# Kernel tuning notes

Measured on AMD Instinct MI355X. Metric: run time of the kernel, lower is better.

The kernel has to match this reference:

```python
import jax, jax.numpy as jnp
import numpy as np

DIM = 768
HEADS = 12
HIDDEN = 3072  # dim * mlp_ratio
EPS = 1e-5


def layernorm(x, g, b):
    mu = jnp.mean(x, axis=-1, keepdims=True)
    var = jnp.var(x, axis=-1, keepdims=True)
    return (x - mu) * jax.lax.rsqrt(var + EPS) * g + b


def setup_inputs() -> dict:
    key = jax.random.key(0)
    ks = jax.random.split(key, 10)
    s = 0.02
    return {
        "x": jax.random.normal(ks[0], (4, 1024, DIM), jnp.float32),
        "attention_mask": jax.random.randint(ks[1], (4, 1024), 0, 2, jnp.int32),
        "ln1_g": jnp.ones((DIM,), jnp.float32),
        "ln1_b": jnp.zeros((DIM,), jnp.float32),
        "ln2_g": jnp.ones((DIM,), jnp.float32),
        "ln2_b": jnp.zeros((DIM,), jnp.float32),
        "w_qkv": jax.random.normal(ks[2], (DIM, 3 * DIM), jnp.float32) * s,
        "b_qkv": jnp.zeros((3 * DIM,), jnp.float32),
        "w_proj": jax.random.normal(ks[3], (DIM, DIM), jnp.float32) * s,
        "b_proj": jnp.zeros((DIM,), jnp.float32),
        "w_fc1": jax.random.normal(ks[4], (DIM, HIDDEN), jnp.float32) * s,
        "b_fc1": jnp.zeros((HIDDEN,), jnp.float32),
        "w_fc2": jax.random.normal(ks[5], (HIDDEN, DIM), jnp.float32) * s,
        "b_fc2": jnp.zeros((DIM,), jnp.float32),
    }


def reference(x, attention_mask, ln1_g, ln1_b, ln2_g, ln2_b,
              w_qkv, b_qkv, w_proj, b_proj, w_fc1, b_fc1, w_fc2, b_fc2):
    B, N, C = x.shape
    hd = C // HEADS
    scale = hd ** -0.5

    # --- attention branch ---
    h = layernorm(x, ln1_g, ln1_b)
    qkv = (h @ w_qkv + b_qkv).reshape(B, N, 3, HEADS, hd)
    q, k, v = qkv[:, :, 0], qkv[:, :, 1], qkv[:, :, 2]  # [B,N,H,hd]
    attn = jnp.einsum('bnhd,bmhd->bhnm', q, k) * scale
    mask_bias = jnp.where(attention_mask == 0, -10000.0, 0.0)[:, None, None, :]
    attn = jax.nn.softmax(attn + mask_bias, axis=-1)
    o = jnp.einsum('bhnm,bmhd->bnhd', attn, v).reshape(B, N, C)
    x = x + (o @ w_proj + b_proj)

    # --- MLP branch ---
    h = layernorm(x, ln2_g, ln2_b)
    h = jax.nn.gelu(h @ w_fc1 + b_fc1, approximate=False)
    x = x + (h @ w_fc2 + b_fc2)
    return x
```

## Files before the change

### kernel.cpp

```cpp
#include <hip/hip_runtime.h>

#define DIM 768
#define NTOK 4096
#define HID 3072

typedef __attribute__((ext_vector_type(8))) short bf16x8;
typedef __attribute__((ext_vector_type(4))) float f32x4;

__device__ inline unsigned short f2bf(float f){
  unsigned u = __float_as_uint(f);
  u += 0x7fff + ((u >> 16) & 1);
  return (unsigned short)(u >> 16);
}
__device__ inline unsigned cvt_pk_bf16(float a, float b){
  unsigned r;
  asm("v_cvt_pk_bf16_f32 %0, %1, %2" : "=v"(r) : "v"(a), "v"(b));
  return r;
}
__device__ inline void gload_lds16(const void* g, void* l){
  __builtin_amdgcn_global_load_lds(
      (const __attribute__((address_space(1))) unsigned int*)g,
      (__attribute__((address_space(3))) unsigned int*)l, 16, 0, 0);
}
template<int N> __device__ inline void wait_vmcnt(){
  if constexpr (N == 0) asm volatile("s_waitcnt vmcnt(0)" ::: "memory");
  else if constexpr (N == 2) asm volatile("s_waitcnt vmcnt(2)" ::: "memory");
  else if constexpr (N == 4) asm volatile("s_waitcnt vmcnt(4)" ::: "memory");
  else if constexpr (N == 6) asm volatile("s_waitcnt vmcnt(6)" ::: "memory");
  else if constexpr (N == 8) asm volatile("s_waitcnt vmcnt(8)" ::: "memory");
  else static_assert(N == 0, "unsupported vmcnt");
}
__device__ inline int swz_read(int row, int hi){
  return (row * 64 + hi * 16) ^ ((row & 7) << 4);
}

__global__ __launch_bounds__(256) void ln_kernel(const float* __restrict__ x,
    const float* __restrict__ g, const float* __restrict__ b,
    unsigned short* __restrict__ out)
{
  int row = blockIdx.x * 4 + (threadIdx.x >> 6);
  int lane = threadIdx.x & 63;
  const float* xr = x + (size_t)row * DIM;
  float4 v[3];
  float s = 0.f, s2 = 0.f;
#pragma unroll
  for (int j = 0; j < 3; ++j){
    v[j] = *(const float4*)(xr + j * 256 + lane * 4);
    s  += v[j].x + v[j].y + v[j].z + v[j].w;
    s2 += v[j].x*v[j].x + v[j].y*v[j].y + v[j].z*v[j].z + v[j].w*v[j].w;
  }
#pragma unroll
  for (int m = 1; m < 64; m <<= 1){ s += __shfl_xor(s, m, 64); s2 += __shfl_xor(s2, m, 64); }
  float mu  = s * (1.f / 768.f);
  float var = s2 * (1.f / 768.f) - mu * mu;
  float inv = rsqrtf(var + 1e-5f);
#pragma unroll
  for (int j = 0; j < 3; ++j){
    int c0 = j * 256 + lane * 4;
    float vv[4] = { v[j].x, v[j].y, v[j].z, v[j].w };
    ushort4 o4;
    o4.x = f2bf((vv[0] - mu) * inv * g[c0 + 0] + b[c0 + 0]);
    o4.y = f2bf((vv[1] - mu) * inv * g[c0 + 1] + b[c0 + 1]);
    o4.z = f2bf((vv[2] - mu) * inv * g[c0 + 2] + b[c0 + 2]);
    o4.w = f2bf((vv[3] - mu) * inv * g[c0 + 3] + b[c0 + 3]);
    *(ushort4*)(out + (size_t)row * DIM + c0) = o4;
  }
}

__global__ __launch_bounds__(256) void transpose4_kernel(
    const float* __restrict__ w_qkv, const float* __restrict__ w_proj,
    const float* __restrict__ w_fc1, const float* __restrict__ w_fc2,
    unsigned short* __restrict__ tq, unsigned short* __restrict__ tp,
    unsigned short* __restrict__ t1, unsigned short* __restrict__ t2)
{
  __shared__ __align__(16) unsigned short tile[32][33];
  int id = blockIdx.x;
  const float* W; unsigned short* Wt; int K, N, tx_n;
  if (id < 1728)      { W = w_qkv;  Wt = tq; K = 768;  N = 2304; tx_n = 72; }
  else if (id < 2304) { W = w_proj; Wt = tp; K = 768;  N = 768;  tx_n = 24; id -= 1728; }
  else if (id < 4608) { W = w_fc1;  Wt = t1; K = 768;  N = 3072; tx_n = 96; id -= 2304; }
  else                { W = w_fc2;  Wt = t2; K = 3072; N = 768;  tx_n = 24; id -= 4608; }
  int n0 = (id % tx_n) * 32, k0 = (id / tx_n) * 32;
  int tx = threadIdx.x & 31, ty = threadIdx.x >> 5;
#pragma unroll
  for (int i = 0; i < 32; i += 8)
    tile[ty + i][tx] = f2bf(W[(size_t)(k0 + ty + i) * N + n0 + tx]);
  __syncthreads();
#pragma unroll
  for (int i = 0; i < 32; i += 8)
    Wt[(size_t)(n0 + ty + i) * K + k0 + tx] = tile[tx][ty + i];
}

__global__ __launch_bounds__(256) void pack_mask_kernel(const int* __restrict__ am,
    unsigned long long* __restrict__ pm)
{
  int lane = threadIdx.x & 63, w = threadIdx.x >> 6, b = blockIdx.x;
  for (int k = w; k < 16; k += 4){
    unsigned long long m = __ballot(am[b * 1024 + k * 64 + lane] != 0);
    if (lane == 0) pm[b * 16 + k] = m;
  }
}

template<int DEPTH, int EPI, typename OutT>
__global__ __launch_bounds__(256) void gemm_kernel(
    const unsigned short* __restrict__ A,
    const unsigned short* __restrict__ Bt,
    const float* __restrict__ bias,
    const float* __restrict__ resid,
    OutT* __restrict__ C,
    unsigned short* __restrict__ q_out,
    unsigned short* __restrict__ k_out,
    unsigned short* __restrict__ v_out,
    int M, int N, int K)
{
  constexpr int BM = 128, BN = 128, BK = 32, WM = 64, WN = 64;
  constexpr int WAVES_N = BN / WN;
  constexpr int MI = WM / 16, NI = WN / 16;
  constexpr int ACH = BM * BK / 8, BCH = BN * BK / 8;
  constexpr int NC = (ACH + BCH) / 256;
  constexpr int SMEM_B = DEPTH * (BM + BN) * BK * 2;
  __shared__ __align__(16) char smem[SMEM_B];
  auto As = (unsigned short(*)[BM * BK])smem;
  auto Bs = (unsigned short(*)[BN * BK])(smem + DEPTH * BM * BK * 2);
  const int t = threadIdx.x, lane = t & 63, wid = t >> 6;
  const int lo = lane & 15, hi = lane >> 4;
  const int wr = wid / WAVES_N, wc = wid % WAVES_N;

  const int gx = gridDim.x;
  const int nwg = gx * gridDim.y;
  const int lin = blockIdx.y * gx + blockIdx.x;
  const int swz = (lin & 7) * (nwg >> 3) + (lin >> 3);
  const int bm = (swz / gx) * BM, bn = (swz % gx) * BN;

  auto stage = [&](int buf, int k0){
#pragma unroll
    for (int u = 0; u < NC; ++u){
      int c = u * 256 + t;
      if (c < ACH){
        int rp = c >> 2, r = rp ^ ((rp >> 2) & 1), q = (c & 3) ^ (r & 3);
        gload_lds16(A + (size_t)(bm + r) * K + k0 + q * 8, &As[buf][c * 8]);
      } else {
        int c2 = c - ACH;
        int rp = c2 >> 2, r = rp ^ ((rp >> 2) & 1), q = (c2 & 3) ^ (r & 3);
        gload_lds16(Bt + (size_t)(bn + r) * K + k0 + q * 8, &Bs[buf][c2 * 8]);
      }
    }
  };

  f32x4 acc[MI][NI];
#pragma unroll
  for (int i = 0; i < MI; ++i)
#pragma unroll
    for (int j = 0; j < NI; ++j) acc[i][j] = (f32x4){0.f, 0.f, 0.f, 0.f};

  const int NIT = K / BK;
#pragma unroll
  for (int d = 0; d < DEPTH - 1; ++d) stage(d, d * BK);
  for (int it = 0; it < NIT; ++it){
    int rem = NIT - 1 - it;
    if (rem >= DEPTH - 2) wait_vmcnt<(DEPTH - 2) * NC>();
    else if (DEPTH == 4 && rem == 1) wait_vmcnt<NC>();
    else wait_vmcnt<0>();
    __builtin_amdgcn_sched_barrier(0);
    __builtin_amdgcn_s_barrier();
    __builtin_amdgcn_sched_barrier(0);
    if (it + DEPTH - 1 < NIT) stage((it + DEPTH - 1) % DEPTH, (it + DEPTH - 1) * BK);
    const char* as = (const char*)As[it % DEPTH];
    const char* bs = (const char*)Bs[it % DEPTH];
    bf16x8 af[MI], bfr[NI];
#pragma unroll
    for (int i = 0; i < MI; ++i){
      int row = wr * WM + i * 16 + lo;
      af[i] = *(const bf16x8*)(as + swz_read(row, hi));
    }
#pragma unroll
    for (int j = 0; j < NI; ++j){
      int row = wc * WN + j * 16 + lo;
      bfr[j] = *(const bf16x8*)(bs + swz_read(row, hi));
    }
#pragma unroll
    for (int i = 0; i < MI; ++i)
#pragma unroll
      for (int j = 0; j < NI; ++j)
        acc[i][j] = __builtin_amdgcn_mfma_f32_16x16x32_bf16(af[i], bfr[j], acc[i][j], 0, 0, 0);
  }

  __syncthreads();

  if constexpr (EPI == 0 || EPI == 1){
    constexpr int LDE = BN + 8;
    unsigned short* ET = (unsigned short*)smem;
#pragma unroll
    for (int i = 0; i < MI; ++i)
#pragma unroll
      for (int j = 0; j < NI; ++j){
        float bcol = bias[bn + wc * WN + j * 16 + lo];
#pragma unroll
        for (int r = 0; r < 4; ++r){
          float v = acc[i][j][r] + bcol;
          if constexpr (EPI == 1) v = 0.5f * v * (1.f + erff(v * 0.70710678118f));
          ET[(wr * WM + i * 16 + hi * 4 + r) * LDE + wc * WN + j * 16 + lo] = f2bf(v);
        }
      }
    __syncthreads();
#pragma unroll
    for (int p = 0; p < BM / 16; ++p){
      int row = p * 16 + (t >> 4), chunk = t & 15;
      *(bf16x8*)&((unsigned short*)C)[(size_t)(bm + row) * N + bn + chunk * 8] =
          *(const bf16x8*)&ET[row * LDE + chunk * 8];
    }
  } else {
    constexpr int LDE = BN + 8;
    unsigned short* ET = (unsigned short*)smem;
    const int part = bn / 768;
    const int cloc = bn % 768;
#pragma unroll
    for (int i = 0; i < MI; ++i)
#pragma unroll
      for (int j = 0; j < NI; ++j){
        int col_l = wc * WN + j * 16 + lo;
        float bcol = bias[bn + col_l];
#pragma unroll
        for (int r = 0; r < 4; ++r){
          int row_l = wr * WM + i * 16 + hi * 4 + r;
          unsigned short us = f2bf(acc[i][j][r] + bcol);
          if (part < 2) ET[row_l * LDE + col_l] = us;
          else          ET[col_l * LDE + row_l] = us;
        }
      }
    __syncthreads();
    const int bb = bm >> 10, n0b = bm & 1023;
    if (part < 2){
      unsigned short* dst0 = (part == 0) ? q_out : k_out;
#pragma unroll
      for (int p = 0; p < 8; ++p){
        int row = p * 16 + (t >> 4), chunk = t & 15;
        int hh = cloc / 64 + (chunk >> 3), d0 = (chunk & 7) * 8;
        unsigned short* dst = dst0 + ((size_t)(bb * 12 + hh)) * 65536 + (n0b + row) * 64 + d0;
        *(bf16x8*)dst = *(const bf16x8*)&ET[row * LDE + chunk * 8];
      }
    } else {
#pragma unroll
      for (int p = 0; p < 8; ++p){
        int colg = p * 16 + (t >> 4), chunk = t & 15;
        int hh = cloc / 64 + (colg >> 6), d = colg & 63;
        unsigned short* dst = v_out + ((size_t)(bb * 12 + hh)) * 65536 + (size_t)d * 1024 + n0b + chunk * 8;
        *(bf16x8*)dst = *(const bf16x8*)&ET[colg * LDE + chunk * 8];
      }
    }
  }
}

template<int DEPTH>
__global__ __launch_bounds__(512) void gemm512_kernel(
    const unsigned short* __restrict__ A,
    const unsigned short* __restrict__ Bt,
    const float* __restrict__ bias,
    const float* __restrict__ resid,
    float* __restrict__ C,
    int M, int N, int K)
{
  constexpr int BM = 128, BN = 96, BK = 32;
  constexpr int MI = 2, NI = 3;
  constexpr int ACH = BM * BK / 8;
  constexpr int BCH = BN * BK / 8;
  constexpr int NC = 2;
  constexpr int SMEM_B = DEPTH * (BM + BN) * BK * 2;
  __shared__ __align__(16) char smem[SMEM_B];
  auto As = (unsigned short(*)[BM * BK])smem;
  auto Bs = (unsigned short(*)[BN * BK])(smem + DEPTH * BM * BK * 2);
  const int t = threadIdx.x, lane = t & 63, wid = t >> 6;
  const int lo = lane & 15, hi = lane >> 4;
  const int wr = wid >> 1, wc = wid & 1;

  const int gx = gridDim.x;
  const int nwg = gx * gridDim.y;
  const int lin = blockIdx.y * gx + blockIdx.x;
  const int swz = (lin & 7) * (nwg >> 3) + (lin >> 3);
  const int bm = (swz / gx) * BM, bn = (swz % gx) * BN;

  auto stage = [&](int buf, int k0){
#pragma unroll
    for (int u = 0; u < NC; ++u){
      int c = u * 512 + t;
      if (c < ACH){
        int rp = c >> 2, r = rp ^ ((rp >> 2) & 1), q = (c & 3) ^ (r & 3);
        gload_lds16(A + (size_t)(bm + r) * K + k0 + q * 8, &As[buf][c * 8]);
      } else {
        int c2 = c - ACH;
        if (c2 >= BCH) c2 -= BCH;
        int rp = c2 >> 2, r = rp ^ ((rp >> 2) & 1), q = (c2 & 3) ^ (r & 3);
        gload_lds16(Bt + (size_t)(bn + r) * K + k0 + q * 8, &Bs[buf][c2 * 8]);
      }
    }
  };

  f32x4 acc[MI][NI];
#pragma unroll
  for (int i = 0; i < MI; ++i)
#pragma unroll
    for (int j = 0; j < NI; ++j) acc[i][j] = (f32x4){0.f, 0.f, 0.f, 0.f};

  const int NIT = K / BK;
#pragma unroll
  for (int d = 0; d < DEPTH - 1; ++d) stage(d, d * BK);
  for (int it = 0; it < NIT; ++it){
    int rem = NIT - 1 - it;
    if (rem >= DEPTH - 2) wait_vmcnt<(DEPTH - 2) * NC>();
    else if (rem == 3)    wait_vmcnt<6>();
    else if (rem == 2)    wait_vmcnt<4>();
    else if (rem == 1)    wait_vmcnt<2>();
    else                  wait_vmcnt<0>();
    __builtin_amdgcn_sched_barrier(0);
    __builtin_amdgcn_s_barrier();
    __builtin_amdgcn_sched_barrier(0);
    if (it + DEPTH - 1 < NIT) stage((it + DEPTH - 1) % DEPTH, (it + DEPTH - 1) * BK);
    const char* as = (const char*)As[it % DEPTH];
    const char* bs = (const char*)Bs[it % DEPTH];
    bf16x8 af[MI], bfr[NI];
#pragma unroll
    for (int i = 0; i < MI; ++i){
      int row = wr * 32 + i * 16 + lo;
      af[i] = *(const bf16x8*)(as + swz_read(row, hi));
    }
#pragma unroll
    for (int j = 0; j < NI; ++j){
      int row = wc * 48 + j * 16 + lo;
      bfr[j] = *(const bf16x8*)(bs + swz_read(row, hi));
    }
#pragma unroll
    for (int i = 0; i < MI; ++i)
#pragma unroll
      for (int j = 0; j < NI; ++j)
        acc[i][j] = __builtin_amdgcn_mfma_f32_16x16x32_bf16(af[i], bfr[j], acc[i][j], 0, 0, 0);
  }

  __syncthreads();
  constexpr int LDE = BN + 4;
  static_assert(BM * LDE * 4 <= SMEM_B, "epilogue tile must fit");
  float* ET = (float*)smem;
#pragma unroll
  for (int i = 0; i < MI; ++i)
#pragma unroll
    for (int j = 0; j < NI; ++j){
      int col_l = wc * 48 + j * 16 + lo;
      float bcol = bias[bn + col_l];
#pragma unroll
      for (int r = 0; r < 4; ++r)
        ET[(wr * 32 + i * 16 + hi * 4 + r) * LDE + col_l] = acc[i][j][r] + bcol;
    }
  __syncthreads();
  {
    int row = t >> 2, q = t & 3;
    const float* rrow = resid + (size_t)(bm + row) * N + bn;
    float* crow = C + (size_t)(bm + row) * N + bn;
#pragma unroll
    for (int k = 0; k < 6; ++k){
      int c4 = (q + k * 4) * 4;
      float4 v = *(const float4*)&ET[row * LDE + c4];
      float4 rs = *(const float4*)&rrow[c4];
      v.x += rs.x; v.y += rs.y; v.z += rs.z; v.w += rs.w;
      *(float4*)&crow[c4] = v;
    }
  }
}

__global__ __launch_bounds__(256) void attn_kernel(
    const unsigned short* __restrict__ Qs,
    const unsigned short* __restrict__ Ks,
    const unsigned short* __restrict__ Vts,
    const unsigned long long* __restrict__ pm,
    unsigned short* __restrict__ o)
{
  constexpr int LD = 72;
  __shared__ __align__(16) unsigned short Kl[64 * LD];
  __shared__ __align__(16) unsigned short Vt[64 * LD];
  __shared__ __align__(16) unsigned short Pl[4][16 * LD];
  const int qb = blockIdx.x, h = blockIdx.y, b = blockIdx.z;
  const int t = threadIdx.x, wid = t >> 6, lane = t & 63;
  const int lo = lane & 15, hi = lane >> 4;
  const size_t bh = (size_t)b * 12 + h;

  const unsigned short* Qg = Qs + (bh * 1024 + qb * 64 + wid * 16 + lo) * 64;
  bf16x8 qf0 = *(const bf16x8*)(Qg + hi * 8);
  bf16x8 qf1 = *(const bf16x8*)(Qg + 32 + hi * 8);

  f32x4 oacc[4];
#pragma unroll
  for (int dj = 0; dj < 4; ++dj) oacc[dj] = (f32x4){0.f, 0.f, 0.f, 0.f};
  float l_part = 0.f;

  const int srow = t >> 2, scol = (t & 3) * 16;
  const unsigned short* Kg = Ks  + bh * 65536;
  const unsigned short* Vg = Vts + bh * 65536;
  unsigned short* pw = &Pl[wid][0];

  for (int kt = 0; kt < 16; ++kt){
    __syncthreads();
    const unsigned short* kg = Kg + (kt * 64 + srow) * 64 + scol;
    *(bf16x8*)&Kl[srow * LD + scol]     = *(const bf16x8*)kg;
    *(bf16x8*)&Kl[srow * LD + scol + 8] = *(const bf16x8*)(kg + 8);
    const unsigned short* vg = Vg + srow * 1024 + kt * 64 + scol;
    *(bf16x8*)&Vt[srow * LD + scol]     = *(const bf16x8*)vg;
    *(bf16x8*)&Vt[srow * LD + scol + 8] = *(const bf16x8*)(vg + 8);
    __syncthreads();

    f32x4 s[4];
#pragma unroll
    for (int nj = 0; nj < 4; ++nj) s[nj] = (f32x4){0.f, 0.f, 0.f, 0.f};
#pragma unroll
    for (int kk = 0; kk < 2; ++kk){
      bf16x8 q = kk ? qf1 : qf0;
#pragma unroll
      for (int nj = 0; nj < 4; ++nj){
        bf16x8 kf = *(const bf16x8*)&Kl[(nj * 16 + lo) * LD + kk * 32 + hi * 8];
        s[nj] = __builtin_amdgcn_mfma_f32_16x16x32_bf16(kf, q, s[nj], 0, 0, 0);
      }
    }

    unsigned long long w = pm[b * 16 + kt] >> (hi * 4);
#pragma unroll
    for (int nj = 0; nj < 4; ++nj){
      float p[4];
#pragma unroll
      for (int r = 0; r < 4; ++r){
        float e = __expf(fmaf(s[nj][r], 0.125f, -16.0f));
        e = ((unsigned)(w >> (nj * 16 + r)) & 1u) ? e : 0.0f;
        l_part += e;
        p[r] = e;
      }
      unsigned w0 = cvt_pk_bf16(p[0], p[1]);
      unsigned w1 = cvt_pk_bf16(p[2], p[3]);
      *(uint2*)&pw[lo * LD + nj * 16 + hi * 4] = make_uint2(w0, w1);
    }
    asm volatile("" ::: "memory");
    bf16x8 pf0 = *(const bf16x8*)&pw[lo * LD + hi * 8];
    bf16x8 pf1 = *(const bf16x8*)&pw[lo * LD + 32 + hi * 8];
#pragma unroll
    for (int kk = 0; kk < 2; ++kk){
      bf16x8 pf = kk ? pf1 : pf0;
#pragma unroll
      for (int dj = 0; dj < 4; ++dj){
        bf16x8 vf = *(const bf16x8*)&Vt[(dj * 16 + lo) * LD + kk * 32 + hi * 8];
        oacc[dj] = __builtin_amdgcn_mfma_f32_16x16x32_bf16(vf, pf, oacc[dj], 0, 0, 0);
      }
    }
  }

  float l = l_part;
  l += __shfl_xor(l, 16, 64);
  l += __shfl_xor(l, 32, 64);
  float inv = 1.0f / l;
  size_t orow = (size_t)b * 1024 + qb * 64 + wid * 16 + lo;
#pragma unroll
  for (int dj = 0; dj < 4; ++dj){
    unsigned w0 = (unsigned)f2bf(oacc[dj][0] * inv) | ((unsigned)f2bf(oacc[dj][1] * inv) << 16);
    unsigned w1 = (unsigned)f2bf(oacc[dj][2] * inv) | ((unsigned)f2bf(oacc[dj][3] * inv) << 16);
    *(uint2*)&o[orow * DIM + h * 64 + dj * 16 + hi * 4] = make_uint2(w0, w1);
  }
}

extern "C" void kernel_launch(void* const* d_in, const int* in_sizes, int n_in,
                              void* d_out, int out_size, void* d_ws, size_t ws_size,
                              hipStream_t stream)
{
  const float* x      = (const float*)d_in[0];
  const int*   amask  = (const int*)  d_in[1];
  const float* ln1_g  = (const float*)d_in[2];
  const float* ln1_b  = (const float*)d_in[3];
  const float* ln2_g  = (const float*)d_in[4];
  const float* ln2_b  = (const float*)d_in[5];
  const float* w_qkv  = (const float*)d_in[6];
  const float* b_qkv  = (const float*)d_in[7];
  const float* w_proj = (const float*)d_in[8];
  const float* b_proj = (const float*)d_in[9];
  const float* w_fc1  = (const float*)d_in[10];
  const float* b_fc1  = (const float*)d_in[11];
  const float* w_fc2  = (const float*)d_in[12];
  const float* b_fc2  = (const float*)d_in[13];
  float* outp = (float*)d_out;

  char* w = (char*)d_ws;
  auto alloc = [&](size_t bytes){ char* p = w; w += (bytes + 255) & ~(size_t)255; return p; };

  char* p0 = alloc((size_t)4 * 6291456);
  unsigned short* Qs   = (unsigned short*)p0;
  unsigned short* Ks   = (unsigned short*)(p0 + 6291456);
  unsigned short* Vts  = (unsigned short*)(p0 + 2 * 6291456);
  unsigned short* o_bf = (unsigned short*)(p0 + 3 * 6291456);
  unsigned short* a1   = (unsigned short*)p0;
  unsigned short* h_bf = (unsigned short*)alloc((size_t)NTOK * DIM * 2);
  unsigned short* h2   = h_bf;
  float*          x1   = (float*)alloc((size_t)NTOK * DIM * 4);
  unsigned short* wqkvT = (unsigned short*)alloc((size_t)3 * DIM * DIM * 2);
  unsigned short* wprojT= (unsigned short*)alloc((size_t)DIM * DIM * 2);
  unsigned short* wfc1T = (unsigned short*)alloc((size_t)HID * DIM * 2);
  unsigned short* wfc2T = (unsigned short*)alloc((size_t)DIM * HID * 2);
  unsigned long long* pmask = (unsigned long long*)alloc(4 * 16 * 8);

  transpose4_kernel<<<6912, 256, 0, stream>>>(w_qkv, w_proj, w_fc1, w_fc2,
                                              wqkvT, wprojT, wfc1T, wfc2T);
  pack_mask_kernel<<<4, 256, 0, stream>>>(amask, pmask);

  ln_kernel<<<NTOK / 4, 256, 0, stream>>>(x, ln1_g, ln1_b, h_bf);
  gemm_kernel<3, 3, unsigned short><<<dim3(2304 / 128, NTOK / 128), 256, 0, stream>>>(
      h_bf, wqkvT, b_qkv, nullptr, (unsigned short*)nullptr, Qs, Ks, Vts, NTOK, 2304, DIM);
  attn_kernel<<<dim3(16, 12, 4), 256, 0, stream>>>(Qs, Ks, Vts, pmask, o_bf);
  gemm512_kernel<4><<<dim3(DIM / 96, NTOK / 128), 512, 0, stream>>>(
      o_bf, wprojT, b_proj, x, x1, NTOK, DIM, DIM);
  ln_kernel<<<NTOK / 4, 256, 0, stream>>>(x1, ln2_g, ln2_b, h2);
  gemm_kernel<3, 1, unsigned short><<<dim3(HID / 128, NTOK / 128), 256, 0, stream>>>(
      h2, wfc1T, b_fc1, nullptr, a1, nullptr, nullptr, nullptr, NTOK, HID, DIM);
  gemm512_kernel<6><<<dim3(DIM / 96, NTOK / 128), 512, 0, stream>>>(
      a1, wfc2T, b_fc2, x1, outp, NTOK, DIM, HID);
}
```

Before: 180.6 us.

## Load B fragments directly to registers in proj/fc2 GEMM, halve M tile

Replaces the 512-thread, 128x96-tile GEMM used for the projection and fc2 with a 256-thread, 64x96-tile kernel. Only A is staged through LDS via async global-to-LDS loads. Each wave loads its B fragments straight from global memory into registers, using a 3-deep register ring unrolled by three. The aim is to cut LDS traffic and barrier cost and to raise the block count for these narrow-N GEMMs, at the cost of more redundant global reads of B and an unswizzled A layout in LDS that may cause bank conflicts. The vmcnt wait scheme is also adjusted for the new load counts, and the now-unused DEPTH==4 case is dropped from the other GEMM.

```diff
diff --git a/kernel.cpp b/kernel.cpp
--- a/kernel.cpp
+++ b/kernel.cpp
@@ -24,9 +24,8 @@
 }
 template<int N> __device__ inline void wait_vmcnt(){
   if constexpr (N == 0) asm volatile("s_waitcnt vmcnt(0)" ::: "memory");
-  else if constexpr (N == 2) asm volatile("s_waitcnt vmcnt(2)" ::: "memory");
   else if constexpr (N == 4) asm volatile("s_waitcnt vmcnt(4)" ::: "memory");
-  else if constexpr (N == 6) asm volatile("s_waitcnt vmcnt(6)" ::: "memory");
+  else if constexpr (N == 7) asm volatile("s_waitcnt vmcnt(7)" ::: "memory");
   else if constexpr (N == 8) asm volatile("s_waitcnt vmcnt(8)" ::: "memory");
   else static_assert(N == 0, "unsupported vmcnt");
 }
@@ -159,7 +158,6 @@
   for (int it = 0; it < NIT; ++it){
     int rem = NIT - 1 - it;
     if (rem >= DEPTH - 2) wait_vmcnt<(DEPTH - 2) * NC>();
-    else if (DEPTH == 4 && rem == 1) wait_vmcnt<NC>();
     else wait_vmcnt<0>();
     __builtin_amdgcn_sched_barrier(0);
     __builtin_amdgcn_s_barrier();
@@ -251,8 +249,7 @@
   }
 }
 
-template<int DEPTH>
-__global__ __launch_bounds__(512) void gemm512_kernel(
+__global__ __launch_bounds__(256) void gemm_bn_kernel(
     const unsigned short* __restrict__ A,
     const unsigned short* __restrict__ Bt,
     const float* __restrict__ bias,
@@ -260,39 +257,25 @@
     float* __restrict__ C,
     int M, int N, int K)
 {
-  constexpr int BM = 128, BN = 96, BK = 32;
+  constexpr int BM = 64, BN = 96, BK = 32;
   constexpr int MI = 2, NI = 3;
-  constexpr int ACH = BM * BK / 8;
-  constexpr int BCH = BN * BK / 8;
-  constexpr int NC = 2;
-  constexpr int SMEM_B = DEPTH * (BM + BN) * BK * 2;
+  constexpr int LDE = BN + 4;
+  constexpr int SMEM_B = (BM * LDE * 4 > 3 * BM * BK * 2) ? BM * LDE * 4 : 3 * BM * BK * 2;
   __shared__ __align__(16) char smem[SMEM_B];
   auto As = (unsigned short(*)[BM * BK])smem;
-  auto Bs = (unsigned short(*)[BN * BK])(smem + DEPTH * BM * BK * 2);
   const int t = threadIdx.x, lane = t & 63, wid = t >> 6;
   const int lo = lane & 15, hi = lane >> 4;
   const int wr = wid >> 1, wc = wid & 1;
-
-  const int gx = gridDim.x;
-  const int nwg = gx * gridDim.y;
-  const int lin = blockIdx.y * gx + blockIdx.x;
-  const int swz = (lin & 7) * (nwg >> 3) + (lin >> 3);
-  const int bm = (swz / gx) * BM, bn = (swz % gx) * BN;
-
-  auto stage = [&](int buf, int k0){
-#pragma unroll
-    for (int u = 0; u < NC; ++u){
-      int c = u * 512 + t;
-      if (c < ACH){
-        int rp = c >> 2, r = rp ^ ((rp >> 2) & 1), q = (c & 3) ^ (r & 3);
-        gload_lds16(A + (size_t)(bm + r) * K + k0 + q * 8, &As[buf][c * 8]);
-      } else {
-        int c2 = c - ACH;
-        if (c2 >= BCH) c2 -= BCH;
-        int rp = c2 >> 2, r = rp ^ ((rp >> 2) & 1), q = (c2 & 3) ^ (r & 3);
-        gload_lds16(Bt + (size_t)(bn + r) * K + k0 + q * 8, &Bs[buf][c2 * 8]);
-      }
-    }
+  const int bm = blockIdx.y * BM, bn = blockIdx.x * BN;
+  const int NIT = K / BK;
+
+  const unsigned short* bptr[NI];
+#pragma unroll
+  for (int j = 0; j < NI; ++j)
+    bptr[j] = Bt + (size_t)(bn + wc * 48 + j * 16 + lo) * K + hi * 8;
+
+  auto stageA = [&](int buf, int k0){
+    gload_lds16(A + (size_t)(bm + (t >> 2)) * K + k0 + (t & 3) * 8, &As[buf][t * 8]);
   };
 
   f32x4 acc[MI][NI];
@@ -301,43 +284,46 @@
 #pragma unroll
     for (int j = 0; j < NI; ++j) acc[i][j] = (f32x4){0.f, 0.f, 0.f, 0.f};
 
-  const int NIT = K / BK;
-#pragma unroll
-  for (int d = 0; d < DEPTH - 1; ++d) stage(d, d * BK);
-  for (int it = 0; it < NIT; ++it){
-    int rem = NIT - 1 - it;
-    if (rem >= DEPTH - 2) wait_vmcnt<(DEPTH - 2) * NC>();
-    else if (rem == 3)    wait_vmcnt<6>();
-    else if (rem == 2)    wait_vmcnt<4>();
-    else if (rem == 1)    wait_vmcnt<2>();
-    else                  wait_vmcnt<0>();
+  bf16x8 b0[NI], b1[NI], b2[NI];
+#pragma unroll
+  for (int j = 0; j < NI; ++j) b0[j] = *(const bf16x8*)(bptr[j]);
+  stageA(0, 0);
+#pragma unroll
+  for (int j = 0; j < NI; ++j) b1[j] = *(const bf16x8*)(bptr[j] + BK);
+  stageA(1, BK);
+
+  auto body = [&](int it, bf16x8 (&bcur)[NI], bf16x8 (&bload)[NI], int rbuf, int wbuf){
+    if (it + 2 < NIT){
+#pragma unroll
+      for (int j = 0; j < NI; ++j)
+        bload[j] = *(const bf16x8*)(bptr[j] + (size_t)(it + 2) * BK);
+    }
+    if (it < NIT - 2) wait_vmcnt<7>();
+    else if (it == NIT - 2) wait_vmcnt<4>();
+    else wait_vmcnt<0>();
     __builtin_amdgcn_sched_barrier(0);
     __builtin_amdgcn_s_barrier();
     __builtin_amdgcn_sched_barrier(0);
-    if (it + DEPTH - 1 < NIT) stage((it + DEPTH - 1) % DEPTH, (it + DEPTH - 1) * BK);
-    const char* as = (const char*)As[it % DEPTH];
-    const char* bs = (const char*)Bs[it % DEPTH];
-    bf16x8 af[MI], bfr[NI];
-#pragma unroll
-    for (int i = 0; i < MI; ++i){
-      int row = wr * 32 + i * 16 + lo;
-      af[i] = *(const bf16x8*)(as + swz_read(row, hi));
-    }
-#pragma unroll
-    for (int j = 0; j < NI; ++j){
-      int row = wc * 48 + j * 16 + lo;
-      bfr[j] = *(const bf16x8*)(bs + swz_read(row, hi));
-    }
+    if (it + 2 < NIT) stageA(wbuf, (it + 2) * BK);
+    const unsigned short* as = As[rbuf];
+    bf16x8 af[MI];
 #pragma unroll
     for (int i = 0; i < MI; ++i)
+      af[i] = *(const bf16x8*)&as[(wr * 32 + i * 16 + lo) * BK + hi * 8];
+#pragma unroll
+    for (int i = 0; i < MI; ++i)
 #pragma unroll
       for (int j = 0; j < NI; ++j)
-        acc[i][j] = __builtin_amdgcn_mfma_f32_16x16x32_bf16(af[i], bfr[j], acc[i][j], 0, 0, 0);
+        acc[i][j] = __builtin_amdgcn_mfma_f32_16x16x32_bf16(af[i], bcur[j], acc[i][j], 0, 0, 0);
+  };
+
+  for (int it = 0; it < NIT; it += 3){
+    body(it,     b0, b2, 0, 2);
+    body(it + 1, b1, b0, 1, 0);
+    body(it + 2, b2, b1, 2, 1);
   }
 
   __syncthreads();
-  constexpr int LDE = BN + 4;
-  static_assert(BM * LDE * 4 <= SMEM_B, "epilogue tile must fit");
   float* ET = (float*)smem;
 #pragma unroll
   for (int i = 0; i < MI; ++i)
@@ -506,11 +492,11 @@
   gemm_kernel<3, 3, unsigned short><<<dim3(2304 / 128, NTOK / 128), 256, 0, stream>>>(
       h_bf, wqkvT, b_qkv, nullptr, (unsigned short*)nullptr, Qs, Ks, Vts, NTOK, 2304, DIM);
   attn_kernel<<<dim3(16, 12, 4), 256, 0, stream>>>(Qs, Ks, Vts, pmask, o_bf);
-  gemm512_kernel<4><<<dim3(DIM / 96, NTOK / 128), 512, 0, stream>>>(
+  gemm_bn_kernel<<<dim3(8, NTOK / 64), 256, 0, stream>>>(
       o_bf, wprojT, b_proj, x, x1, NTOK, DIM, DIM);
   ln_kernel<<<NTOK / 4, 256, 0, stream>>>(x1, ln2_g, ln2_b, h2);
   gemm_kernel<3, 1, unsigned short><<<dim3(HID / 128, NTOK / 128), 256, 0, stream>>>(
       h2, wfc1T, b_fc1, nullptr, a1, nullptr, nullptr, nullptr, NTOK, HID, DIM);
-  gemm512_kernel<6><<<dim3(DIM / 96, NTOK / 128), 512, 0, stream>>>(
+  gemm_bn_kernel<<<dim3(8, NTOK / 64), 256, 0, stream>>>(
       a1, wfc2T, b_fc2, x1, outp, NTOK, DIM, HID);
 }
```

New measurement: 227.1 us. 25.8% more time.

## Split K across wave pairs in the narrow-N GEMMs with BK=64 tiles

Applied to the files above, without the earlier changes.

Replaces the 512-thread projection/fc2 GEMM with a variant in which pairs of waves each take half of a 64-wide K slice. Each wave now covers a 64x48 output block, and the two partial sums are combined through LDS in the epilogue. It also changes the swizzle to 8-chunk rows, uses a fixed 3-deep pipeline, and drops the unused resid parameter from the other GEMM. The goal is more MFMA work per LDS read and fewer barriers per K step. In exchange it doubles accumulator registers and adds an LDS reduction pass.

```diff
diff --git a/kernel.cpp b/kernel.cpp
--- a/kernel.cpp
+++ b/kernel.cpp
@@ -24,9 +24,7 @@
 }
 template<int N> __device__ inline void wait_vmcnt(){
   if constexpr (N == 0) asm volatile("s_waitcnt vmcnt(0)" ::: "memory");
-  else if constexpr (N == 2) asm volatile("s_waitcnt vmcnt(2)" ::: "memory");
   else if constexpr (N == 4) asm volatile("s_waitcnt vmcnt(4)" ::: "memory");
-  else if constexpr (N == 6) asm volatile("s_waitcnt vmcnt(6)" ::: "memory");
   else if constexpr (N == 8) asm volatile("s_waitcnt vmcnt(8)" ::: "memory");
   else static_assert(N == 0, "unsupported vmcnt");
 }
@@ -106,7 +104,6 @@
     const unsigned short* __restrict__ A,
     const unsigned short* __restrict__ Bt,
     const float* __restrict__ bias,
-    const float* __restrict__ resid,
     OutT* __restrict__ C,
     unsigned short* __restrict__ q_out,
     unsigned short* __restrict__ k_out,
@@ -159,7 +156,6 @@
   for (int it = 0; it < NIT; ++it){
     int rem = NIT - 1 - it;
     if (rem >= DEPTH - 2) wait_vmcnt<(DEPTH - 2) * NC>();
-    else if (DEPTH == 4 && rem == 1) wait_vmcnt<NC>();
     else wait_vmcnt<0>();
     __builtin_amdgcn_sched_barrier(0);
     __builtin_amdgcn_s_barrier();
@@ -251,8 +247,7 @@
   }
 }
 
-template<int DEPTH>
-__global__ __launch_bounds__(512) void gemm512_kernel(
+__global__ __launch_bounds__(512) void gemm_ks_kernel(
     const unsigned short* __restrict__ A,
     const unsigned short* __restrict__ Bt,
     const float* __restrict__ bias,
@@ -260,18 +255,21 @@
     float* __restrict__ C,
     int M, int N, int K)
 {
-  constexpr int BM = 128, BN = 96, BK = 32;
-  constexpr int MI = 2, NI = 3;
+  constexpr int BM = 128, BN = 96, BK = 64, DEPTH = 3;
+  constexpr int MI = 4, NI = 3;
   constexpr int ACH = BM * BK / 8;
   constexpr int BCH = BN * BK / 8;
-  constexpr int NC = 2;
-  constexpr int SMEM_B = DEPTH * (BM + BN) * BK * 2;
+  constexpr int NC = 4;
+  constexpr int TILE_A = BM * BK * 2, TILE_B = BN * BK * 2;
+  constexpr int LDE = BN + 4;
+  constexpr int SMEM_B = (DEPTH * (TILE_A + TILE_B) > BM * LDE * 4)
+                       ?  DEPTH * (TILE_A + TILE_B) : BM * LDE * 4;
   __shared__ __align__(16) char smem[SMEM_B];
   auto As = (unsigned short(*)[BM * BK])smem;
-  auto Bs = (unsigned short(*)[BN * BK])(smem + DEPTH * BM * BK * 2);
+  auto Bs = (unsigned short(*)[BN * BK])(smem + DEPTH * TILE_A);
   const int t = threadIdx.x, lane = t & 63, wid = t >> 6;
   const int lo = lane & 15, hi = lane >> 4;
-  const int wr = wid >> 1, wc = wid & 1;
+  const int ks = wid & 1, wc = (wid >> 1) & 1, wr = wid >> 2;
 
   const int gx = gridDim.x;
   const int nwg = gx * gridDim.y;
@@ -284,16 +282,19 @@
     for (int u = 0; u < NC; ++u){
       int c = u * 512 + t;
       if (c < ACH){
-        int rp = c >> 2, r = rp ^ ((rp >> 2) & 1), q = (c & 3) ^ (r & 3);
+        int r = c >> 3, q = (c & 7) ^ (r & 7);
         gload_lds16(A + (size_t)(bm + r) * K + k0 + q * 8, &As[buf][c * 8]);
       } else {
         int c2 = c - ACH;
         if (c2 >= BCH) c2 -= BCH;
-        int rp = c2 >> 2, r = rp ^ ((rp >> 2) & 1), q = (c2 & 3) ^ (r & 3);
+        int r = c2 >> 3, q = (c2 & 7) ^ (r & 7);
         gload_lds16(Bt + (size_t)(bn + r) * K + k0 + q * 8, &Bs[buf][c2 * 8]);
       }
     }
   };
+  auto rd = [&](const char* base, int row, int q)->bf16x8 {
+    return *(const bf16x8*)(base + row * 128 + ((q ^ (row & 7)) << 4));
+  };
 
   f32x4 acc[MI][NI];
 #pragma unroll
@@ -302,32 +303,23 @@
     for (int j = 0; j < NI; ++j) acc[i][j] = (f32x4){0.f, 0.f, 0.f, 0.f};
 
   const int NIT = K / BK;
-#pragma unroll
-  for (int d = 0; d < DEPTH - 1; ++d) stage(d, d * BK);
+  stage(0, 0);
+  stage(1, BK);
+  const int qk = ks * 4 + hi;
   for (int it = 0; it < NIT; ++it){
-    int rem = NIT - 1 - it;
-    if (rem >= DEPTH - 2) wait_vmcnt<(DEPTH - 2) * NC>();
-    else if (rem == 3)    wait_vmcnt<6>();
-    else if (rem == 2)    wait_vmcnt<4>();
-    else if (rem == 1)    wait_vmcnt<2>();
-    else                  wait_vmcnt<0>();
+    if (it < NIT - 1) wait_vmcnt<NC>();
+    else wait_vmcnt<0>();
     __builtin_amdgcn_sched_barrier(0);
     __builtin_amdgcn_s_barrier();
     __builtin_amdgcn_sched_barrier(0);
-    if (it + DEPTH - 1 < NIT) stage((it + DEPTH - 1) % DEPTH, (it + DEPTH - 1) * BK);
+    if (it + 2 < NIT) stage((it + 2) % DEPTH, (it + 2) * BK);
     const char* as = (const char*)As[it % DEPTH];
     const char* bs = (const char*)Bs[it % DEPTH];
     bf16x8 af[MI], bfr[NI];
 #pragma unroll
-    for (int i = 0; i < MI; ++i){
-      int row = wr * 32 + i * 16 + lo;
-      af[i] = *(const bf16x8*)(as + swz_read(row, hi));
-    }
-#pragma unroll
-    for (int j = 0; j < NI; ++j){
-      int row = wc * 48 + j * 16 + lo;
-      bfr[j] = *(const bf16x8*)(bs + swz_read(row, hi));
-    }
+    for (int i = 0; i < MI; ++i)  af[i]  = rd(as, wr * 64 + i * 16 + lo, qk);
+#pragma unroll
+    for (int j = 0; j < NI; ++j) bfr[j] = rd(bs, wc * 48 + j * 16 + lo, qk);
 #pragma unroll
     for (int i = 0; i < MI; ++i)
 #pragma unroll
@@ -336,19 +328,31 @@
   }
 
   __syncthreads();
-  constexpr int LDE = BN + 4;
-  static_assert(BM * LDE * 4 <= SMEM_B, "epilogue tile must fit");
   float* ET = (float*)smem;
-#pragma unroll
-  for (int i = 0; i < MI; ++i)
-#pragma unroll
-    for (int j = 0; j < NI; ++j){
-      int col_l = wc * 48 + j * 16 + lo;
-      float bcol = bias[bn + col_l];
-#pragma unroll
-      for (int r = 0; r < 4; ++r)
-        ET[(wr * 32 + i * 16 + hi * 4 + r) * LDE + col_l] = acc[i][j][r] + bcol;
-    }
+  if (ks == 1){
+#pragma unroll
+    for (int i = 0; i < MI; ++i)
+#pragma unroll
+      for (int j = 0; j < NI; ++j)
+#pragma unroll
+        for (int r = 0; r < 4; ++r)
+          ET[(wr * 64 + i * 16 + hi * 4 + r) * LDE + wc * 48 + j * 16 + lo] = acc[i][j][r];
+  }
+  __syncthreads();
+  if (ks == 0){
+#pragma unroll
+    for (int i = 0; i < MI; ++i)
+#pragma unroll
+      for (int j = 0; j < NI; ++j){
+        int col_l = wc * 48 + j * 16 + lo;
+        float bcol = bias[bn + col_l];
+#pragma unroll
+        for (int r = 0; r < 4; ++r){
+          int idx = (wr * 64 + i * 16 + hi * 4 + r) * LDE + col_l;
+          ET[idx] = ET[idx] + acc[i][j][r] + bcol;
+        }
+      }
+  }
   __syncthreads();
   {
     int row = t >> 2, q = t & 3;
@@ -504,13 +508,13 @@
 
   ln_kernel<<<NTOK / 4, 256, 0, stream>>>(x, ln1_g, ln1_b, h_bf);
   gemm_kernel<3, 3, unsigned short><<<dim3(2304 / 128, NTOK / 128), 256, 0, stream>>>(
-      h_bf, wqkvT, b_qkv, nullptr, (unsigned short*)nullptr, Qs, Ks, Vts, NTOK, 2304, DIM);
+      h_bf, wqkvT, b_qkv, (unsigned short*)nullptr, Qs, Ks, Vts, NTOK, 2304, DIM);
   attn_kernel<<<dim3(16, 12, 4), 256, 0, stream>>>(Qs, Ks, Vts, pmask, o_bf);
-  gemm512_kernel<4><<<dim3(DIM / 96, NTOK / 128), 512, 0, stream>>>(
+  gemm_ks_kernel<<<dim3(8, NTOK / 128), 512, 0, stream>>>(
       o_bf, wprojT, b_proj, x, x1, NTOK, DIM, DIM);
   ln_kernel<<<NTOK / 4, 256, 0, stream>>>(x1, ln2_g, ln2_b, h2);
   gemm_kernel<3, 1, unsigned short><<<dim3(HID / 128, NTOK / 128), 256, 0, stream>>>(
-      h2, wfc1T, b_fc1, nullptr, a1, nullptr, nullptr, nullptr, NTOK, HID, DIM);
-  gemm512_kernel<6><<<dim3(DIM / 96, NTOK / 128), 512, 0, stream>>>(
+      h2, wfc1T, b_fc1, a1, nullptr, nullptr, nullptr, NTOK, HID, DIM);
+  gemm_ks_kernel<<<dim3(8, NTOK / 128), 512, 0, stream>>>(
       a1, wfc2T, b_fc2, x1, outp, NTOK, DIM, HID);
 }
```

Result: faster. 169.0 us (-6.4%).
